# Kernel optimization log

Measured on AMD Instinct MI355X. Metric: run time of the kernel, lower is better.

The kernel has to match this reference:

```python
import jax, jax.numpy as jnp
import numpy as np

N_MESH = 128
BOX_SIZE = 12.8
SPACING = BOX_SIZE / N_MESH  # 0.1
N_POINTS = 100000
N_CHANNELS = 16


def setup_inputs() -> dict:
    key = jax.random.key(0)
    k1, k2 = jax.random.split(key)
    mesh_values = jax.random.normal(k1, (N_CHANNELS, N_MESH, N_MESH, N_MESH), dtype=jnp.float32)
    points = jax.random.uniform(k2, (N_POINTS, 3), dtype=jnp.float32) * BOX_SIZE
    return {"mesh_values": mesh_values, "points": points}


def reference(mesh_values, points):
    # points in real space -> fractional grid coordinates
    pc = points / SPACING                       # [N, 3]
    rp = jnp.round(pc).astype(jnp.int32)        # nearest grid point [N, 3]
    dist = pc - rp.astype(pc.dtype)             # [N, 3], in [-0.5, 0.5]
    # quadratic (order-3) interpolation weights for offsets -1, 0, +1
    w_m = (2.0 * dist - 1.0) ** 2 / 8.0
    w_0 = 0.75 - dist * dist
    w_p = (2.0 * dist + 1.0) ** 2 / 8.0
    w = jnp.stack([w_m, w_0, w_p], axis=0)      # [3, N, 3] (offset, point, axis)
    # periodic-wrapped indices for offsets -1, 0, +1
    idx = (rp[None, :, :] + jnp.array([-1, 0, 1], dtype=jnp.int32)[:, None, None]) % N_MESH  # [3, N, 3]
    # all 27 offset combinations
    ox, oy, oz = jnp.meshgrid(jnp.arange(3), jnp.arange(3), jnp.arange(3), indexing="ij")
    ox, oy, oz = ox.ravel(), oy.ravel(), oz.ravel()  # [27]
    ix = idx[ox, :, 0]  # [27, N]
    iy = idx[oy, :, 1]
    iz = idx[oz, :, 2]
    lin = (ix * N_MESH + iy) * N_MESH + iz      # [27, N] linear mesh index
    gathered = mesh_values.reshape(N_CHANNELS, -1)[:, lin]   # [C, 27, N]
    weight = w[ox, :, 0] * w[oy, :, 1] * w[oz, :, 2]          # [27, N]
    out = jnp.einsum("con,on->nc", gathered, weight)          # [N, C]
    return out
```

## Files before the change

kernel.cpp:

```cpp
#include <hip/hip_runtime.h>
#include <hip/hip_fp16.h>

#define NMESH 128
#define NMESH2 (128 * 128)
#define NMESH3 (128 * 128 * 128)
#define NPOINTS 100000
#define NCH 16

__global__ __launch_bounds__(256) void transpose_to_half_v2(
    const float* __restrict__ in,
    __half* __restrict__ outT)
{
    const int s = blockIdx.x * 256 + threadIdx.x;

    float v[NCH];
#pragma unroll
    for (int c = 0; c < NCH; ++c)
        v[c] = in[(size_t)c * NMESH3 + s];

    uint32_t u[8];
#pragma unroll
    for (int k = 0; k < 8; ++k) {
        u[k] = (uint32_t)__half_as_ushort(__float2half(v[2 * k])) |
               ((uint32_t)__half_as_ushort(__float2half(v[2 * k + 1])) << 16);
    }

    uint4* dst = (uint4*)(outT + (size_t)s * NCH);
    dst[0] = make_uint4(u[0], u[1], u[2], u[3]);
    dst[1] = make_uint4(u[4], u[5], u[6], u[7]);
}

__global__ __launch_bounds__(256) void gather_half_v2(
    const __half* __restrict__ meshT,
    const float* __restrict__ pts,
    float* __restrict__ out)
{
    const int tid = blockIdx.x * 256 + threadIdx.x;
    const int p = tid >> 2;
    const int c0 = (tid & 3) * 4;
    if (p >= NPOINTS) return;

    const float SP = 0.1f;
    const float pcx = pts[p * 3 + 0] / SP;
    const float pcy = pts[p * 3 + 1] / SP;
    const float pcz = pts[p * 3 + 2] / SP;

    const int rx = (int)rintf(pcx);
    const int ry = (int)rintf(pcy);
    const int rz = (int)rintf(pcz);

    const float dx = pcx - (float)rx;
    const float dy = pcy - (float)ry;
    const float dz = pcz - (float)rz;

    float wX[3], wY[3], wZ[3];
    wX[0] = (2.0f * dx - 1.0f) * (2.0f * dx - 1.0f) * 0.125f;
    wX[1] = 0.75f - dx * dx;
    wX[2] = (2.0f * dx + 1.0f) * (2.0f * dx + 1.0f) * 0.125f;
    wY[0] = (2.0f * dy - 1.0f) * (2.0f * dy - 1.0f) * 0.125f;
    wY[1] = 0.75f - dy * dy;
    wY[2] = (2.0f * dy + 1.0f) * (2.0f * dy + 1.0f) * 0.125f;
    wZ[0] = (2.0f * dz - 1.0f) * (2.0f * dz - 1.0f) * 0.125f;
    wZ[1] = 0.75f - dz * dz;
    wZ[2] = (2.0f * dz + 1.0f) * (2.0f * dz + 1.0f) * 0.125f;

    int xo[3], yo[3], zo[3];
#pragma unroll
    for (int k = 0; k < 3; ++k) {
        xo[k] = ((rx - 1 + k) & (NMESH - 1)) * (NMESH2 * NCH);
        yo[k] = ((ry - 1 + k) & (NMESH - 1)) * (NMESH * NCH);
        zo[k] = ((rz - 1 + k) & (NMESH - 1)) * NCH + c0;
    }

    float acc0 = 0.0f, acc1 = 0.0f, acc2 = 0.0f, acc3 = 0.0f;
#pragma unroll
    for (int a = 0; a < 3; ++a) {
#pragma unroll
        for (int b = 0; b < 3; ++b) {
            const int base = xo[a] + yo[b];
            const float wxy = wX[a] * wY[b];
#pragma unroll
            for (int k = 0; k < 3; ++k) {
                const float2 raw = *(const float2*)(meshT + base + zo[k]);
                const __half2 h01 = *(const __half2*)&raw.x;
                const __half2 h23 = *(const __half2*)&raw.y;
                const float2 f01 = __half22float2(h01);
                const float2 f23 = __half22float2(h23);
                const float w = wxy * wZ[k];
                acc0 = fmaf(f01.x, w, acc0);
                acc1 = fmaf(f01.y, w, acc1);
                acc2 = fmaf(f23.x, w, acc2);
                acc3 = fmaf(f23.y, w, acc3);
            }
        }
    }

    float4 res = make_float4(acc0, acc1, acc2, acc3);
    *(float4*)(out + (size_t)p * NCH + c0) = res;
}

__global__ __launch_bounds__(256) void mesh_interp_fallback_kernel(
    const float* __restrict__ mesh,
    const float* __restrict__ pts,
    float* __restrict__ out)
{
    const int tid = blockIdx.x * 256 + threadIdx.x;
    const int c = tid & (NCH - 1);
    const int p = tid >> 4;
    if (p >= NPOINTS) return;

    const float SP = 0.1f;
    const float pcx = pts[p * 3 + 0] / SP;
    const float pcy = pts[p * 3 + 1] / SP;
    const float pcz = pts[p * 3 + 2] / SP;

    const int rx = (int)rintf(pcx);
    const int ry = (int)rintf(pcy);
    const int rz = (int)rintf(pcz);

    const float dx = pcx - (float)rx;
    const float dy = pcy - (float)ry;
    const float dz = pcz - (float)rz;

    float wX[3], wY[3], wZ[3];
    wX[0] = (2.0f * dx - 1.0f) * (2.0f * dx - 1.0f) * 0.125f;
    wX[1] = 0.75f - dx * dx;
    wX[2] = (2.0f * dx + 1.0f) * (2.0f * dx + 1.0f) * 0.125f;
    wY[0] = (2.0f * dy - 1.0f) * (2.0f * dy - 1.0f) * 0.125f;
    wY[1] = 0.75f - dy * dy;
    wY[2] = (2.0f * dy + 1.0f) * (2.0f * dy + 1.0f) * 0.125f;
    wZ[0] = (2.0f * dz - 1.0f) * (2.0f * dz - 1.0f) * 0.125f;
    wZ[1] = 0.75f - dz * dz;
    wZ[2] = (2.0f * dz + 1.0f) * (2.0f * dz + 1.0f) * 0.125f;

    int xb[3], yb[3], zi[3];
#pragma unroll
    for (int k = 0; k < 3; ++k) {
        xb[k] = ((rx - 1 + k) & (NMESH - 1)) * NMESH2;
        yb[k] = ((ry - 1 + k) & (NMESH - 1)) * NMESH;
        zi[k] = ((rz - 1 + k) & (NMESH - 1));
    }

    const float* __restrict__ mc = mesh + (size_t)c * NMESH3;
    float acc = 0.0f;
#pragma unroll
    for (int a = 0; a < 3; ++a) {
#pragma unroll
        for (int b = 0; b < 3; ++b) {
            const float* __restrict__ row = mc + xb[a] + yb[b];
            const float wxy = wX[a] * wY[b];
            acc = fmaf(row[zi[0]], wxy * wZ[0], acc);
            acc = fmaf(row[zi[1]], wxy * wZ[1], acc);
            acc = fmaf(row[zi[2]], wxy * wZ[2], acc);
        }
    }
    out[tid] = acc;
}

extern "C" void kernel_launch(void* const* d_in, const int* in_sizes, int n_in,
                              void* d_out, int out_size, void* d_ws, size_t ws_size,
                              hipStream_t stream) {
    const float* mesh = (const float*)d_in[0];
    const float* pts  = (const float*)d_in[1];
    float* out        = (float*)d_out;

    const size_t needed = (size_t)NMESH3 * NCH * sizeof(__half);

    if (ws_size >= needed) {
        __half* meshT = (__half*)d_ws;
        transpose_to_half_v2<<<NMESH3 / 256, 256, 0, stream>>>(mesh, meshT);
        const int total = NPOINTS * 4;
        gather_half_v2<<<(total + 255) / 256, 256, 0, stream>>>(meshT, pts, out);
    } else {
        const int total = NPOINTS * NCH;
        mesh_interp_fallback_kernel<<<(total + 255) / 256, 256, 0, stream>>>(mesh, pts, out);
    }
}
```

Before: 226.7 us.

## Bin-sort points by spatial cell before gathering from half-precision mesh

Result: slower. 241.9 us (+6.7%).

```diff
diff --git a/kernel.cpp b/kernel.cpp
--- a/kernel.cpp
+++ b/kernel.cpp
@@ -6,10 +6,24 @@
 #define NMESH3 (128 * 128 * 128)
 #define NPOINTS 100000
 #define NCH 16
+#define NBINS 4096
+
+#define WS_MESHT_OFF   0
+#define WS_COUNTS_OFF  (64u * 1024u * 1024u)
+#define WS_OFFSETS_OFF (WS_COUNTS_OFF + 16384u)
+#define WS_SORTED_OFF  (WS_OFFSETS_OFF + 16384u)
+#define WS_NEEDED      (WS_SORTED_OFF + (size_t)NPOINTS * 16u)
+
+__device__ __forceinline__ void cell_of_point(const float px, const float py,
+                                              const float pz, int& rx, int& ry, int& rz) {
+    const float SP = 0.1f;
+    rx = (int)rintf(px / SP);
+    ry = (int)rintf(py / SP);
+    rz = (int)rintf(pz / SP);
+}
 
 __global__ __launch_bounds__(256) void transpose_to_half_v2(
-    const float* __restrict__ in,
-    __half* __restrict__ outT)
+    const float* __restrict__ in, __half* __restrict__ outT)
 {
     const int s = blockIdx.x * 256 + threadIdx.x;
 
@@ -30,20 +44,92 @@
     dst[1] = make_uint4(u[4], u[5], u[6], u[7]);
 }
 
-__global__ __launch_bounds__(256) void gather_half_v2(
+__global__ __launch_bounds__(256) void zero_counts_kernel(int* __restrict__ counts) {
+    const int t = threadIdx.x;
+#pragma unroll
+    for (int k = 0; k < NBINS / 256; ++k) counts[t + 256 * k] = 0;
+}
+
+__device__ __forceinline__ int bin_of_cell(int rx, int ry, int rz) {
+    const int bx = (rx & (NMESH - 1)) >> 3;
+    const int by = (ry & (NMESH - 1)) >> 3;
+    const int bz = (rz & (NMESH - 1)) >> 3;
+    return (bx * 16 + by) * 16 + bz;
+}
+
+__global__ __launch_bounds__(256) void histogram_kernel(
+    const float* __restrict__ pts, int* __restrict__ counts)
+{
+    const int p = blockIdx.x * 256 + threadIdx.x;
+    if (p >= NPOINTS) return;
+    int rx, ry, rz;
+    cell_of_point(pts[p * 3 + 0], pts[p * 3 + 1], pts[p * 3 + 2], rx, ry, rz);
+    atomicAdd(&counts[bin_of_cell(rx, ry, rz)], 1);
+}
+
+__global__ __launch_bounds__(256) void scan_kernel(
+    const int* __restrict__ counts, int* __restrict__ offsets)
+{
+    __shared__ int s[256];
+    const int t = threadIdx.x;
+    const int base = t * (NBINS / 256);
+
+    int local[NBINS / 256];
+    int total = 0;
+#pragma unroll
+    for (int i = 0; i < NBINS / 256; ++i) {
+        local[i] = counts[base + i];
+        total += local[i];
+    }
+    s[t] = total;
+    __syncthreads();
+
+    for (int off = 1; off < 256; off <<= 1) {
+        int v = (t >= off) ? s[t - off] : 0;
+        __syncthreads();
+        s[t] += v;
+        __syncthreads();
+    }
+    int running = s[t] - total;
+#pragma unroll
+    for (int i = 0; i < NBINS / 256; ++i) {
+        offsets[base + i] = running;
+        running += local[i];
+    }
+}
+
+__global__ __launch_bounds__(256) void scatter_kernel(
+    const float* __restrict__ pts, int* __restrict__ offsets,
+    float4* __restrict__ sorted)
+{
+    const int p = blockIdx.x * 256 + threadIdx.x;
+    if (p >= NPOINTS) return;
+    const float px = pts[p * 3 + 0];
+    const float py = pts[p * 3 + 1];
+    const float pz = pts[p * 3 + 2];
+    int rx, ry, rz;
+    cell_of_point(px, py, pz, rx, ry, rz);
+    const int pos = atomicAdd(&offsets[bin_of_cell(rx, ry, rz)], 1);
+    sorted[pos] = make_float4(px, py, pz, __int_as_float(p));
+}
+
+__global__ __launch_bounds__(256) void gather_sorted_kernel(
     const __half* __restrict__ meshT,
-    const float* __restrict__ pts,
+    const float4* __restrict__ sorted,
     float* __restrict__ out)
 {
     const int tid = blockIdx.x * 256 + threadIdx.x;
-    const int p = tid >> 2;
+    const int si = tid >> 2;
     const int c0 = (tid & 3) * 4;
-    if (p >= NPOINTS) return;
+    if (si >= NPOINTS) return;
+
+    const float4 sp = sorted[si];
+    const int orig = __float_as_int(sp.w);
 
     const float SP = 0.1f;
-    const float pcx = pts[p * 3 + 0] / SP;
-    const float pcy = pts[p * 3 + 1] / SP;
-    const float pcz = pts[p * 3 + 2] / SP;
+    const float pcx = sp.x / SP;
+    const float pcy = sp.y / SP;
+    const float pcz = sp.z / SP;
 
     const int rx = (int)rintf(pcx);
     const int ry = (int)rintf(pcy);
@@ -95,8 +181,7 @@
         }
     }
 
-    float4 res = make_float4(acc0, acc1, acc2, acc3);
-    *(float4*)(out + (size_t)p * NCH + c0) = res;
+    *(float4*)(out + (size_t)orig * NCH + c0) = make_float4(acc0, acc1, acc2, acc3);
 }
 
 __global__ __launch_bounds__(256) void mesh_interp_fallback_kernel(
@@ -164,15 +249,20 @@
     const float* pts  = (const float*)d_in[1];
     float* out        = (float*)d_out;
 
-    const size_t needed = (size_t)NMESH3 * NCH * sizeof(__half);
-
-    if (ws_size >= needed) {
-        __half* meshT = (__half*)d_ws;
+    if (ws_size >= WS_NEEDED) {
+        char* ws = (char*)d_ws;
+        __half* meshT   = (__half*)(ws + WS_MESHT_OFF);
+        int*    counts  = (int*)(ws + WS_COUNTS_OFF);
+        int*    offsets = (int*)(ws + WS_OFFSETS_OFF);
+        float4* sorted  = (float4*)(ws + WS_SORTED_OFF);
+
         transpose_to_half_v2<<<NMESH3 / 256, 256, 0, stream>>>(mesh, meshT);
-        const int total = NPOINTS * 4;
-        gather_half_v2<<<(total + 255) / 256, 256, 0, stream>>>(meshT, pts, out);
+        zero_counts_kernel<<<1, 256, 0, stream>>>(counts);
+        histogram_kernel<<<(NPOINTS + 255) / 256, 256, 0, stream>>>(pts, counts);
+        scan_kernel<<<1, 256, 0, stream>>>(counts, offsets);
+        scatter_kernel<<<(NPOINTS + 255) / 256, 256, 0, stream>>>(pts, offsets, sorted);
+        gather_sorted_kernel<<<(NPOINTS * 4 + 255) / 256, 256, 0, stream>>>(meshT, sorted, out);
     } else {
-        const int total = NPOINTS * NCH;
-        mesh_interp_fallback_kernel<<<(total + 255) / 256, 256, 0, stream>>>(mesh, pts, out);
-    }
-}
+        mesh_interp_fallback_kernel<<<(NPOINTS * NCH + 255) / 256, 256, 0, stream>>>(mesh, pts, out);
+    }
+}
```
